# Kernel optimization log

Hardware: AMD Instinct MI355X
Metric: run time of the kernel (lower is better)

Reference implementation:

```python
import jax, jax.numpy as jnp
import numpy as np

C = 256
DQK = C // 8


def setup_inputs() -> dict:
    key = jax.random.key(0)
    ks = jax.random.split(key, 7)
    B, H, W = 8, 64, 64
    x = jax.random.normal(ks[0], (B, H, W, C), dtype=jnp.float32)
    # 1x1 conv weights (equivalent to per-pixel dense): [Cin, Cout] + bias
    sq = 1.0 / np.sqrt(C)
    Wq = jax.random.normal(ks[1], (C, DQK), dtype=jnp.float32) * sq
    bq = jnp.zeros((DQK,), dtype=jnp.float32)
    Wk = jax.random.normal(ks[2], (C, DQK), dtype=jnp.float32) * sq
    bk = jnp.zeros((DQK,), dtype=jnp.float32)
    Wv = jax.random.normal(ks[3], (C, C), dtype=jnp.float32) * sq
    bv = jnp.zeros((C,), dtype=jnp.float32)
    gamma = jnp.float32(0.5)  # nonzero so attention path affects output/grads
    return {"x": x, "Wq": Wq, "bq": bq, "Wk": Wk, "bk": bk,
            "Wv": Wv, "bv": bv, "gamma": gamma}


def reference(x, Wq, bq, Wk, bk, Wv, bv, gamma):
    B, H, W, c = x.shape
    n = H * W
    xf = x.reshape(B, n, c)                      # [B, hw, C]
    q = xf @ Wq + bq                              # [B, hw, C//8]
    k = xf @ Wk + bk                              # [B, hw, C//8]
    v = xf @ Wv + bv                              # [B, hw, C]
    scores = jnp.einsum('bnd,bmd->bnm', q, k)     # [B, hw, hw], no scaling (faithful)
    attn = jax.nn.softmax(scores, axis=-1)
    out = jnp.einsum('bnm,bmc->bnc', attn, v)     # [B, hw, C]
    out = out.reshape(B, H, W, c)
    return gamma * out + x
```

## Files before the change

### kernel.cpp

```cpp
#include <hip/hip_runtime.h>
#include <hip/hip_bf16.h>
#include <math.h>

#define B_ 8
#define N_ 4096
#define C_ 256
#define DQK_ 32

typedef float f32x4  __attribute__((ext_vector_type(4)));
typedef float f32x16 __attribute__((ext_vector_type(16)));
typedef short bf16x8 __attribute__((ext_vector_type(8)));
typedef short bf16x4 __attribute__((ext_vector_type(4)));

__device__ __forceinline__ short f2bf(float f){
  union { float f; unsigned u; } v; v.f = f;
  unsigned r = v.u + 0x7fffu + ((v.u >> 16) & 1u);
  return (short)(r >> 16);
}

__global__ void cast_wt_kernel(const float* __restrict__ Wq, const float* __restrict__ Wk,
                               const float* __restrict__ Wv, short* __restrict__ WT){
  int n = blockIdx.x;
  int k = threadIdx.x;
  float val;
  if (n < 32)       val = Wq[k*32 + n];
  else if (n < 64)  val = Wk[k*32 + (n-32)];
  else              val = Wv[k*256 + (n-64)];
  WT[n*256 + k] = f2bf(val);
}

__global__ __launch_bounds__(256) void proj_kernel(
    const float* __restrict__ x, const short* __restrict__ WT,
    const float* __restrict__ bq, const float* __restrict__ bk, const float* __restrict__ bv,
    short* __restrict__ qws, short* __restrict__ kws, short* __restrict__ vSw){
  __shared__ __align__(16) short sX[64*264];
  __shared__ __align__(16) short sT[64*72];
  int tid = threadIdx.x;
  int lane = tid & 63, wave = tid >> 6;
  int lane15 = lane & 15, quad = lane >> 4;
  int mbase = blockIdx.x * 64;
  int b = mbase >> 12, kvb = mbase & (N_-1);

  const float* xr = x + (size_t)mbase * C_;
  for (int i = 0; i < 8; i++){
    int s = tid + i*256;
    int row = s >> 5, cg = (s & 31) << 3;
    const f32x4* src = (const f32x4*)(xr + row*C_ + cg);
    f32x4 a = src[0], c = src[1];
    bf16x8 p;
    p[0]=f2bf(a[0]); p[1]=f2bf(a[1]); p[2]=f2bf(a[2]); p[3]=f2bf(a[3]);
    p[4]=f2bf(c[0]); p[5]=f2bf(c[1]); p[6]=f2bf(c[2]); p[7]=f2bf(c[3]);
    *(bf16x8*)(sX + row*264 + cg) = p;
  }
  __syncthreads();

  f32x4 acc[5][4];
  for (int i=0;i<5;i++) for (int mt=0;mt<4;mt++) acc[i][mt] = (f32x4)(0.f);

  for (int kc = 0; kc < 8; kc++){
    bf16x8 afr[4];
    #pragma unroll
    for (int mt=0;mt<4;mt++)
      afr[mt] = *(const bf16x8*)(sX + (mt*16+lane15)*264 + kc*32 + quad*8);
    bf16x8 bfr[5];
    #pragma unroll
    for (int i=0;i<5;i++){
      int t = i*4 + wave;
      bfr[i] = *(const bf16x8*)(WT + (size_t)(t*16+lane15)*256 + kc*32 + quad*8);
    }
    #pragma unroll
    for (int i=0;i<5;i++)
      #pragma unroll
      for (int mt=0;mt<4;mt++)
        acc[i][mt] = __builtin_amdgcn_mfma_f32_16x16x32_bf16(afr[mt], bfr[i], acc[i][mt], 0,0,0);
  }

  #pragma unroll
  for (int i=0;i<5;i++){
    int t = i*4 + wave;
    int n0 = t*16 + lane15;
    float bias = (n0 < 32) ? bq[n0] : (n0 < 64 ? bk[n0-32] : bv[n0-64]);
    if (n0 < 64){
      #pragma unroll
      for (int mt=0;mt<4;mt++)
        #pragma unroll
        for (int r=0;r<4;r++)
          sT[(mt*16 + quad*4 + r)*72 + n0] = f2bf(acc[i][mt][r] + bias);
    } else {
      int ch = n0 - 64, cht = ch >> 5, c5 = ch & 31;
      int lanep = c5 | ((quad & 1) << 5);
      int jo = (quad >> 1) * 4;
      #pragma unroll
      for (int mt=0;mt<4;mt++){
        bf16x4 pk;
        pk[0]=f2bf(acc[i][mt][0]+bias); pk[1]=f2bf(acc[i][mt][1]+bias);
        pk[2]=f2bf(acc[i][mt][2]+bias); pk[3]=f2bf(acc[i][mt][3]+bias);
        size_t off = (size_t)b*1048576 + (size_t)(kvb>>6)*16384
                   + (size_t)(mt*8 + cht)*512 + (size_t)lanep*8 + jo;
        *(bf16x4*)(vSw + off) = pk;
      }
    }
  }
  __syncthreads();

  {
    int qt = tid >> 7, p = (tid >> 6) & 1, ln = tid & 63;
    int row = qt*32 + (ln & 31);
    int dcol = p*16 + (ln >> 5)*8;
    bf16x8 vq = *(const bf16x8*)(sT + row*72 + dcol);
    bf16x8 vk = *(const bf16x8*)(sT + row*72 + 32 + dcol);
    size_t qoff = ((((size_t)b*128 + ((kvb>>5) + qt))*2 + p)*64 + ln)*8;
    *(bf16x8*)(qws + qoff) = vq;
    size_t koff = ((size_t)b*64 + (kvb>>6))*2048 + (size_t)((qt*2 + p)*64 + ln)*8;
    *(bf16x8*)(kws + koff) = vk;
  }
}

__global__ __launch_bounds__(512, 2) void flash_kernel(
    const float* __restrict__ x, const short* __restrict__ qws, const short* __restrict__ kws,
    const short* __restrict__ vSw, const float* __restrict__ gptr, float* __restrict__ out){
  __shared__ __align__(16) char smem[98304];
  short* sV0 = (short*)smem;
  short* sV1 = (short*)(smem + 32768);
  int tid = threadIdx.x;
  int lane = tid & 63, wave = tid >> 6;
  int l31 = lane & 31, h = lane >> 5;
  int qt = wave >> 1, kh = wave & 1;
  int b = blockIdx.x & 7;
  int q0 = (blockIdx.x >> 3) << 7;

  const short* qb = qws + (size_t)b*131072;
  const short* kb = kws + (size_t)b*131072;
  const short* vb = vSw + (size_t)b*1048576;

  int qtg = (q0 >> 5) + qt;
  bf16x8 qf0 = *(const bf16x8*)(qb + (size_t)((qtg*2+0)*64 + lane)*8);
  bf16x8 qf1 = *(const bf16x8*)(qb + (size_t)((qtg*2+1)*64 + lane)*8);

  const short* kf0p = kb + (size_t)((2*kh+0)*64 + lane)*8;
  const short* kf1p = kb + (size_t)((2*kh+1)*64 + lane)*8;
  bf16x8 kfc0 = *(const bf16x8*)(kf0p);
  bf16x8 kfc1 = *(const bf16x8*)(kf1p);
  bf16x8 kfn0 = kfc0, kfn1 = kfc1;

  #pragma unroll
  for (int r=0;r<4;r++)
    __builtin_amdgcn_global_load_lds(
      (const __attribute__((address_space(1))) void*)(vb + (size_t)(r*512+tid)*8),
      (__attribute__((address_space(3))) void*)(sV0 + (size_t)(r*512+tid)*8), 16, 0, 0);
  __syncthreads();

  f32x16 acc[8], accl;
  #pragma unroll
  for (int t=0;t<8;t++) acc[t] = (f32x16)(0.f);
  accl = (f32x16)(0.f);
  bf16x8 ones;
  #pragma unroll
  for (int j=0;j<8;j++) ones[j] = (short)0x3F80;

  for (int it=0; it<64; it++){
    short* sVc = (it & 1) ? sV1 : sV0;
    short* sVn = (it & 1) ? sV0 : sV1;
    if (it < 63){
      const short* vsrc = vb + (size_t)(it+1)*16384;
      #pragma unroll
      for (int r=0;r<4;r++)
        __builtin_amdgcn_global_load_lds(
          (const __attribute__((address_space(1))) void*)(vsrc + (size_t)(r*512+tid)*8),
          (__attribute__((address_space(3))) void*)(sVn + (size_t)(r*512+tid)*8), 16, 0, 0);
      kfn0 = *(const bf16x8*)(kf0p + (size_t)(it+1)*2048);
      kfn1 = *(const bf16x8*)(kf1p + (size_t)(it+1)*2048);
    }

    f32x16 s = __builtin_amdgcn_mfma_f32_32x32x16_bf16(kfc0, qf0, (f32x16)(0.f), 0,0,0);
    s        = __builtin_amdgcn_mfma_f32_32x32x16_bf16(kfc1, qf1, s, 0,0,0);

    bf16x8 pf[2];
    #pragma unroll
    for (int g=0; g<2; g++){
      union { bf16x8 v; unsigned u[4]; } P;
      #pragma unroll
      for (int j=0;j<4;j++){
        float2 e;
        e.x = __expf(s[g*8 + 2*j]);
        e.y = __expf(s[g*8 + 2*j + 1]);
        __hip_bfloat162 t2 = __float22bfloat162_rn(e);
        __builtin_memcpy(&P.u[j], &t2, 4);
      }
      pf[g] = P.v;
    }

    #pragma unroll
    for (int g=0; g<2; g++){
      const short* base = sVc + (2*kh + g)*4096;
      #pragma unroll
      for (int cht=0; cht<8; cht++){
        bf16x8 vf = *(const bf16x8*)(base + (cht*64 + lane)*8);
        acc[cht] = __builtin_amdgcn_mfma_f32_32x32x16_bf16(pf[g], vf, acc[cht], 0,0,0);
      }
      accl = __builtin_amdgcn_mfma_f32_32x32x16_bf16(pf[g], ones, accl, 0,0,0);
    }
    kfc0 = kfn0; kfc1 = kfn1;
    __syncthreads();
  }

  float* R1 = (float*)smem;
  float* RL = (float*)(smem + 65536);
  int pw = wave ^ 1;
  if (kh == 0){
    #pragma unroll
    for (int i=0;i<16;i++){ R1[wave*2048 + i*64 + lane] = acc[4][i];
                            R1[wave*2048 + 1024 + i*64 + lane] = acc[5][i]; }
  } else {
    #pragma unroll
    for (int i=0;i<16;i++){ R1[wave*2048 + i*64 + lane] = acc[0][i];
                            R1[wave*2048 + 1024 + i*64 + lane] = acc[1][i]; }
  }
  #pragma unroll
  for (int i=0;i<16;i++) RL[wave*1024 + i*64 + lane] = accl[i];
  __syncthreads();
  if (kh == 0){
    #pragma unroll
    for (int i=0;i<16;i++){ acc[0][i] += R1[pw*2048 + i*64 + lane];
                            acc[1][i] += R1[pw*2048 + 1024 + i*64 + lane]; }
  } else {
    #pragma unroll
    for (int i=0;i<16;i++){ acc[4][i] += R1[pw*2048 + i*64 + lane];
                            acc[5][i] += R1[pw*2048 + 1024 + i*64 + lane]; }
  }
  #pragma unroll
  for (int i=0;i<16;i++) accl[i] += RL[pw*1024 + i*64 + lane];
  __syncthreads();
  if (kh == 0){
    #pragma unroll
    for (int i=0;i<16;i++){ R1[wave*2048 + i*64 + lane] = acc[6][i];
                            R1[wave*2048 + 1024 + i*64 + lane] = acc[7][i]; }
  } else {
    #pragma unroll
    for (int i=0;i<16;i++){ R1[wave*2048 + i*64 + lane] = acc[2][i];
                            R1[wave*2048 + 1024 + i*64 + lane] = acc[3][i]; }
  }
  __syncthreads();
  if (kh == 0){
    #pragma unroll
    for (int i=0;i<16;i++){ acc[2][i] += R1[pw*2048 + i*64 + lane];
                            acc[3][i] += R1[pw*2048 + 1024 + i*64 + lane]; }
  } else {
    #pragma unroll
    for (int i=0;i<16;i++){ acc[6][i] += R1[pw*2048 + i*64 + lane];
                            acc[7][i] += R1[pw*2048 + 1024 + i*64 + lane]; }
  }

  float g = *gptr;
  const float* xb = x + ((size_t)b*N_ + q0 + qt*32)*C_;
  float*       ob = out + ((size_t)b*N_ + q0 + qt*32)*C_;
  if (kh == 0){
    #pragma unroll
    for (int i=0;i<16;i++){
      int q = (i&3) + 8*(i>>2) + 4*h;
      float rv = 1.f / accl[i];
      #pragma unroll
      for (int ct=0; ct<4; ct++){
        int ch = ct*32 + l31;
        ob[(size_t)q*C_ + ch] = g*(acc[ct][i]*rv) + xb[(size_t)q*C_ + ch];
      }
    }
  } else {
    #pragma unroll
    for (int i=0;i<16;i++){
      int q = (i&3) + 8*(i>>2) + 4*h;
      float rv = 1.f / accl[i];
      #pragma unroll
      for (int ct=0; ct<4; ct++){
        int ch = (4+ct)*32 + l31;
        ob[(size_t)q*C_ + ch] = g*(acc[4+ct][i]*rv) + xb[(size_t)q*C_ + ch];
      }
    }
  }
}

extern "C" void kernel_launch(void* const* d_in, const int* in_sizes, int n_in,
                              void* d_out, int out_size, void* d_ws, size_t ws_size,
                              hipStream_t stream){
  const float* x  = (const float*)d_in[0];
  const float* Wq = (const float*)d_in[1];
  const float* bq = (const float*)d_in[2];
  const float* Wk = (const float*)d_in[3];
  const float* bk = (const float*)d_in[4];
  const float* Wv = (const float*)d_in[5];
  const float* bv = (const float*)d_in[6];
  const float* gm = (const float*)d_in[7];
  float* out = (float*)d_out;
  char* ws = (char*)d_ws;
  short* WT  = (short*)ws;
  short* qws = (short*)(ws + 163840);
  short* kws = (short*)(ws + 163840 + 2097152);
  short* vSw = (short*)(ws + 163840 + 2*2097152);

  cast_wt_kernel<<<dim3(320), dim3(256), 0, stream>>>(Wq, Wk, Wv, WT);
  proj_kernel<<<dim3(512), dim3(256), 0, stream>>>(x, WT, bq, bk, bv, qws, kws, vSw);
  flash_kernel<<<dim3(256), dim3(512), 0, stream>>>(x, qws, kws, vSw, gm, out);
}
```

Measured before the change: 188.6 us.

## Software-pipeline QK scores one step ahead and compute row sums on VALU

Unrolls the KV loop by two with explicit ping-pong buffers so the next tile's QK^T MFMAs are issued alongside the current tile's exp and PV MFMAs. It also drops the extra MFMA against a ones vector, accumulating softmax row sums in scalar registers and reducing them through a small shared table. Shared memory shrinks to about 65 KB, which may help occupancy. The cost is more live registers and more complex control flow. The row-sum mapping relies on the MFMA output lane layout, where each lane's s values belong to a single query column.

```diff
diff --git a/kernel.cpp b/kernel.cpp
--- a/kernel.cpp
+++ b/kernel.cpp
@@ -119,7 +119,7 @@
 __global__ __launch_bounds__(512, 2) void flash_kernel(
     const float* __restrict__ x, const short* __restrict__ qws, const short* __restrict__ kws,
     const short* __restrict__ vSw, const float* __restrict__ gptr, float* __restrict__ out){
-  __shared__ __align__(16) char smem[98304];
+  __shared__ __align__(16) char smem[66560];
   short* sV0 = (short*)smem;
   short* sV1 = (short*)(smem + 32768);
   int tid = threadIdx.x;
@@ -139,74 +139,103 @@
 
   const short* kf0p = kb + (size_t)((2*kh+0)*64 + lane)*8;
   const short* kf1p = kb + (size_t)((2*kh+1)*64 + lane)*8;
-  bf16x8 kfc0 = *(const bf16x8*)(kf0p);
-  bf16x8 kfc1 = *(const bf16x8*)(kf1p);
-  bf16x8 kfn0 = kfc0, kfn1 = kfc1;
-
-  #pragma unroll
-  for (int r=0;r<4;r++)
-    __builtin_amdgcn_global_load_lds(
-      (const __attribute__((address_space(1))) void*)(vb + (size_t)(r*512+tid)*8),
-      (__attribute__((address_space(3))) void*)(sV0 + (size_t)(r*512+tid)*8), 16, 0, 0);
-  __syncthreads();
-
-  f32x16 acc[8], accl;
+  bf16x8 kA0 = *(const bf16x8*)(kf0p);
+  bf16x8 kA1 = *(const bf16x8*)(kf1p);
+  bf16x8 kB0 = *(const bf16x8*)(kf0p + 2048);
+  bf16x8 kB1 = *(const bf16x8*)(kf1p + 2048);
+
+#define VPREF(CHUNK, DST) do { \
+    const short* vsrc_ = vb + (size_t)(CHUNK)*16384; \
+    _Pragma("unroll") \
+    for (int r_=0;r_<4;r_++) \
+      __builtin_amdgcn_global_load_lds( \
+        (const __attribute__((address_space(1))) void*)(vsrc_ + (size_t)(r_*512+tid)*8), \
+        (__attribute__((address_space(3))) void*)((DST) + (size_t)(r_*512+tid)*8), 16, 0, 0); \
+  } while(0)
+
+#define QKS(K0, K1) ({ \
+    f32x16 t_ = __builtin_amdgcn_mfma_f32_32x32x16_bf16((K0), qf0, (f32x16)(0.f), 0,0,0); \
+    __builtin_amdgcn_mfma_f32_32x32x16_bf16((K1), qf1, t_, 0,0,0); })
+
+#define EXPPACK(S, PF) do { \
+    float ls_ = 0.f; \
+    _Pragma("unroll") \
+    for (int g_=0; g_<2; g_++){ \
+      union { bf16x8 v; unsigned u[4]; } P_; \
+      _Pragma("unroll") \
+      for (int j_=0;j_<4;j_++){ \
+        float2 e_; \
+        e_.x = __expf((S)[g_*8 + 2*j_]); \
+        e_.y = __expf((S)[g_*8 + 2*j_ + 1]); \
+        ls_ += e_.x + e_.y; \
+        __hip_bfloat162 t2_ = __float22bfloat162_rn(e_); \
+        __builtin_memcpy(&P_.u[j_], &t2_, 4); \
+      } \
+      (PF)[g_] = P_.v; \
+    } \
+    rsum += ls_; \
+  } while(0)
+
+#define PV_STEP(SVC, PF) do { \
+    _Pragma("unroll") \
+    for (int g_=0; g_<2; g_++){ \
+      const short* base_ = (SVC) + (2*kh + g_)*4096; \
+      _Pragma("unroll") \
+      for (int cht_=0; cht_<8; cht_++){ \
+        bf16x8 vf_ = *(const bf16x8*)(base_ + (cht_*64 + lane)*8); \
+        acc[cht_] = __builtin_amdgcn_mfma_f32_32x32x16_bf16((PF)[g_], vf_, acc[cht_], 0,0,0); \
+      } \
+    } \
+  } while(0)
+
+  VPREF(0, sV0);
+  __syncthreads();
+
+  f32x16 acc[8];
   #pragma unroll
   for (int t=0;t<8;t++) acc[t] = (f32x16)(0.f);
-  accl = (f32x16)(0.f);
-  bf16x8 ones;
-  #pragma unroll
-  for (int j=0;j<8;j++) ones[j] = (short)0x3F80;
-
-  for (int it=0; it<64; it++){
-    short* sVc = (it & 1) ? sV1 : sV0;
-    short* sVn = (it & 1) ? sV0 : sV1;
-    if (it < 63){
-      const short* vsrc = vb + (size_t)(it+1)*16384;
-      #pragma unroll
-      for (int r=0;r<4;r++)
-        __builtin_amdgcn_global_load_lds(
-          (const __attribute__((address_space(1))) void*)(vsrc + (size_t)(r*512+tid)*8),
-          (__attribute__((address_space(3))) void*)(sVn + (size_t)(r*512+tid)*8), 16, 0, 0);
-      kfn0 = *(const bf16x8*)(kf0p + (size_t)(it+1)*2048);
-      kfn1 = *(const bf16x8*)(kf1p + (size_t)(it+1)*2048);
-    }
-
-    f32x16 s = __builtin_amdgcn_mfma_f32_32x32x16_bf16(kfc0, qf0, (f32x16)(0.f), 0,0,0);
-    s        = __builtin_amdgcn_mfma_f32_32x32x16_bf16(kfc1, qf1, s, 0,0,0);
-
-    bf16x8 pf[2];
-    #pragma unroll
-    for (int g=0; g<2; g++){
-      union { bf16x8 v; unsigned u[4]; } P;
-      #pragma unroll
-      for (int j=0;j<4;j++){
-        float2 e;
-        e.x = __expf(s[g*8 + 2*j]);
-        e.y = __expf(s[g*8 + 2*j + 1]);
-        __hip_bfloat162 t2 = __float22bfloat162_rn(e);
-        __builtin_memcpy(&P.u[j], &t2, 4);
-      }
-      pf[g] = P.v;
-    }
-
-    #pragma unroll
-    for (int g=0; g<2; g++){
-      const short* base = sVc + (2*kh + g)*4096;
-      #pragma unroll
-      for (int cht=0; cht<8; cht++){
-        bf16x8 vf = *(const bf16x8*)(base + (cht*64 + lane)*8);
-        acc[cht] = __builtin_amdgcn_mfma_f32_32x32x16_bf16(pf[g], vf, acc[cht], 0,0,0);
-      }
-      accl = __builtin_amdgcn_mfma_f32_32x32x16_bf16(pf[g], ones, accl, 0,0,0);
-    }
-    kfc0 = kfn0; kfc1 = kfn1;
-    __syncthreads();
+  float rsum = 0.f;
+
+  f32x16 s0 = QKS(kA0, kA1);
+  f32x16 s1 = (f32x16)(0.f);
+  kA0 = *(const bf16x8*)(kf0p + 2*2048);
+  kA1 = *(const bf16x8*)(kf1p + 2*2048);
+
+  for (int it2 = 0; it2 < 32; it2++){
+    {
+      VPREF(2*it2+1, sV1);
+      bf16x8 pf[2];
+      EXPPACK(s0, pf);
+      s1 = QKS(kB0, kB1);
+      if (it2 < 31){
+        kB0 = *(const bf16x8*)(kf0p + (size_t)(2*it2+3)*2048);
+        kB1 = *(const bf16x8*)(kf1p + (size_t)(2*it2+3)*2048);
+      }
+      PV_STEP(sV0, pf);
+      __syncthreads();
+    }
+    {
+      if (it2 < 31) VPREF(2*it2+2, sV0);
+      bf16x8 pf[2];
+      EXPPACK(s1, pf);
+      if (it2 < 31){
+        s0 = QKS(kA0, kA1);
+        if (it2 < 30){
+          kA0 = *(const bf16x8*)(kf0p + (size_t)(2*it2+4)*2048);
+          kA1 = *(const bf16x8*)(kf1p + (size_t)(2*it2+4)*2048);
+        }
+      }
+      PV_STEP(sV1, pf);
+      __syncthreads();
+    }
   }
 
   float* R1 = (float*)smem;
-  float* RL = (float*)(smem + 65536);
+  float* TAB = (float*)(smem + 65536);
   int pw = wave ^ 1;
+  rsum += __shfl_xor(rsum, 32);
+  if (lane < 32) TAB[wave*32 + lane] = rsum;
+
   if (kh == 0){
     #pragma unroll
     for (int i=0;i<16;i++){ R1[wave*2048 + i*64 + lane] = acc[4][i];
@@ -216,8 +245,6 @@
     for (int i=0;i<16;i++){ R1[wave*2048 + i*64 + lane] = acc[0][i];
                             R1[wave*2048 + 1024 + i*64 + lane] = acc[1][i]; }
   }
-  #pragma unroll
-  for (int i=0;i<16;i++) RL[wave*1024 + i*64 + lane] = accl[i];
   __syncthreads();
   if (kh == 0){
     #pragma unroll
@@ -228,8 +255,6 @@
     for (int i=0;i<16;i++){ acc[4][i] += R1[pw*2048 + i*64 + lane];
                             acc[5][i] += R1[pw*2048 + 1024 + i*64 + lane]; }
   }
-  #pragma unroll
-  for (int i=0;i<16;i++) accl[i] += RL[pw*1024 + i*64 + lane];
   __syncthreads();
   if (kh == 0){
     #pragma unroll
@@ -258,7 +283,7 @@
     #pragma unroll
     for (int i=0;i<16;i++){
       int q = (i&3) + 8*(i>>2) + 4*h;
-      float rv = 1.f / accl[i];
+      float rv = 1.f / (TAB[(qt*2+0)*32 + q] + TAB[(qt*2+1)*32 + q]);
       #pragma unroll
       for (int ct=0; ct<4; ct++){
         int ch = ct*32 + l31;
@@ -269,7 +294,7 @@
     #pragma unroll
     for (int i=0;i<16;i++){
       int q = (i&3) + 8*(i>>2) + 4*h;
-      float rv = 1.f / accl[i];
+      float rv = 1.f / (TAB[(qt*2+0)*32 + q] + TAB[(qt*2+1)*32 + q]);
       #pragma unroll
       for (int ct=0; ct<4; ct++){
         int ch = (4+ct)*32 + l31;
@@ -277,6 +302,10 @@
       }
     }
   }
+#undef VPREF
+#undef QKS
+#undef EXPPACK
+#undef PV_STEP
 }
 
 extern "C" void kernel_launch(void* const* d_in, const int* in_sizes, int n_in,
```

Measured after the change: 191.6 us. No clear change (+1.6%).

## Deepen V prefetch to four LDS buffers and compute row sums in VALU

Applied to the files above, without the earlier changes.

Changes the V staging from a double buffer to a four-slot LDS ring with a two-iteration prefetch distance. Each iteration now waits with a manual vmcnt and one raw s_barrier instead of a full __syncthreads. The softmax denominator is no longer an extra MFMA against a ones vector; it is accumulated as a scalar sum of the exponentials, reduced across lanes and waves in LDS, which removes two MFMAs per iteration. The LDS footprint grows to 128KB per block, which may cut occupancy below the two blocks per CU that launch_bounds asks for. The hand-tuned vmcnt counts could also be fragile.

```diff
diff --git a/kernel.cpp b/kernel.cpp
--- a/kernel.cpp
+++ b/kernel.cpp
@@ -119,9 +119,7 @@
 __global__ __launch_bounds__(512, 2) void flash_kernel(
     const float* __restrict__ x, const short* __restrict__ qws, const short* __restrict__ kws,
     const short* __restrict__ vSw, const float* __restrict__ gptr, float* __restrict__ out){
-  __shared__ __align__(16) char smem[98304];
-  short* sV0 = (short*)smem;
-  short* sV1 = (short*)(smem + 32768);
+  __shared__ __align__(16) char smem[131072];
   int tid = threadIdx.x;
   int lane = tid & 63, wave = tid >> 6;
   int l31 = lane & 31, h = lane >> 5;
@@ -139,42 +137,41 @@
 
   const short* kf0p = kb + (size_t)((2*kh+0)*64 + lane)*8;
   const short* kf1p = kb + (size_t)((2*kh+1)*64 + lane)*8;
+
+#define VPREF(CHUNK, DST) do { \
+    const short* vsrc_ = vb + (size_t)(CHUNK)*16384; \
+    _Pragma("unroll") \
+    for (int r_=0;r_<4;r_++) \
+      __builtin_amdgcn_global_load_lds( \
+        (const __attribute__((address_space(1))) void*)(vsrc_ + (size_t)(r_*512+tid)*8), \
+        (__attribute__((address_space(3))) void*)((DST) + (size_t)(r_*512+tid)*8), 16, 0, 0); \
+  } while(0)
+
+  VPREF(0, (short*)smem);
+  VPREF(1, (short*)(smem + 32768));
+  __builtin_amdgcn_sched_barrier(0);
   bf16x8 kfc0 = *(const bf16x8*)(kf0p);
   bf16x8 kfc1 = *(const bf16x8*)(kf1p);
-  bf16x8 kfn0 = kfc0, kfn1 = kfc1;
-
-  #pragma unroll
-  for (int r=0;r<4;r++)
-    __builtin_amdgcn_global_load_lds(
-      (const __attribute__((address_space(1))) void*)(vb + (size_t)(r*512+tid)*8),
-      (__attribute__((address_space(3))) void*)(sV0 + (size_t)(r*512+tid)*8), 16, 0, 0);
-  __syncthreads();
-
-  f32x16 acc[8], accl;
+  __builtin_amdgcn_sched_barrier(0);
+  bf16x8 kfn0, kfn1;
+
+  f32x16 acc[8];
   #pragma unroll
   for (int t=0;t<8;t++) acc[t] = (f32x16)(0.f);
-  accl = (f32x16)(0.f);
-  bf16x8 ones;
-  #pragma unroll
-  for (int j=0;j<8;j++) ones[j] = (short)0x3F80;
+  float rsO = 0.f;
 
   for (int it=0; it<64; it++){
-    short* sVc = (it & 1) ? sV1 : sV0;
-    short* sVn = (it & 1) ? sV0 : sV1;
-    if (it < 63){
-      const short* vsrc = vb + (size_t)(it+1)*16384;
-      #pragma unroll
-      for (int r=0;r<4;r++)
-        __builtin_amdgcn_global_load_lds(
-          (const __attribute__((address_space(1))) void*)(vsrc + (size_t)(r*512+tid)*8),
-          (__attribute__((address_space(3))) void*)(sVn + (size_t)(r*512+tid)*8), 16, 0, 0);
-      kfn0 = *(const bf16x8*)(kf0p + (size_t)(it+1)*2048);
-      kfn1 = *(const bf16x8*)(kf1p + (size_t)(it+1)*2048);
-    }
+    int nk = (it+1 < 64) ? (it+1) : 63;
+    int ns = (it+2 < 64) ? (it+2) : 63;
+
+    kfn0 = *(const bf16x8*)(kf0p + (size_t)nk*2048);
+    kfn1 = *(const bf16x8*)(kf1p + (size_t)nk*2048);
+    __builtin_amdgcn_sched_barrier(0);
+    VPREF(ns, (short*)(smem + ((size_t)((it+2)&3))*32768));
+    __builtin_amdgcn_sched_barrier(0);
 
     f32x16 s = __builtin_amdgcn_mfma_f32_32x32x16_bf16(kfc0, qf0, (f32x16)(0.f), 0,0,0);
     s        = __builtin_amdgcn_mfma_f32_32x32x16_bf16(kfc1, qf1, s, 0,0,0);
-
     bf16x8 pf[2];
     #pragma unroll
     for (int g=0; g<2; g++){
@@ -184,29 +181,44 @@
         float2 e;
         e.x = __expf(s[g*8 + 2*j]);
         e.y = __expf(s[g*8 + 2*j + 1]);
+        rsO += e.x + e.y;
         __hip_bfloat162 t2 = __float22bfloat162_rn(e);
         __builtin_memcpy(&P.u[j], &t2, 4);
       }
       pf[g] = P.v;
     }
 
-    #pragma unroll
-    for (int g=0; g<2; g++){
-      const short* base = sVc + (2*kh + g)*4096;
-      #pragma unroll
-      for (int cht=0; cht<8; cht++){
-        bf16x8 vf = *(const bf16x8*)(base + (cht*64 + lane)*8);
-        acc[cht] = __builtin_amdgcn_mfma_f32_32x32x16_bf16(pf[g], vf, acc[cht], 0,0,0);
-      }
-      accl = __builtin_amdgcn_mfma_f32_32x32x16_bf16(pf[g], ones, accl, 0,0,0);
+    asm volatile("s_waitcnt vmcnt(4)" ::: "memory");
+    __builtin_amdgcn_sched_barrier(0);
+    __builtin_amdgcn_s_barrier();
+    __builtin_amdgcn_sched_barrier(0);
+
+    {
+      const short* sVc = (const short*)(smem + ((size_t)(it&3))*32768);
+      #pragma unroll
+      for (int g=0; g<2; g++){
+        const short* base = sVc + (2*kh + g)*4096;
+        #pragma unroll
+        for (int cht=0; cht<8; cht++){
+          bf16x8 vf = *(const bf16x8*)(base + (cht*64 + lane)*8);
+          acc[cht] = __builtin_amdgcn_mfma_f32_32x32x16_bf16(pf[g], vf, acc[cht], 0,0,0);
+        }
+      }
     }
     kfc0 = kfn0; kfc1 = kfn1;
-    __syncthreads();
-  }
-
+  }
+
+  asm volatile("s_waitcnt vmcnt(0)" ::: "memory");
+  __builtin_amdgcn_sched_barrier(0);
+  __builtin_amdgcn_s_barrier();
+  __builtin_amdgcn_sched_barrier(0);
+
+  rsO += __shfl_xor(rsO, 32);
   float* R1 = (float*)smem;
-  float* RL = (float*)(smem + 65536);
+  float* RS = (float*)(smem + 65536);
   int pw = wave ^ 1;
+  if (lane < 32) RS[wave*32 + l31] = rsO;
+
   if (kh == 0){
     #pragma unroll
     for (int i=0;i<16;i++){ R1[wave*2048 + i*64 + lane] = acc[4][i];
@@ -216,8 +228,6 @@
     for (int i=0;i<16;i++){ R1[wave*2048 + i*64 + lane] = acc[0][i];
                             R1[wave*2048 + 1024 + i*64 + lane] = acc[1][i]; }
   }
-  #pragma unroll
-  for (int i=0;i<16;i++) RL[wave*1024 + i*64 + lane] = accl[i];
   __syncthreads();
   if (kh == 0){
     #pragma unroll
@@ -228,8 +238,6 @@
     for (int i=0;i<16;i++){ acc[4][i] += R1[pw*2048 + i*64 + lane];
                             acc[5][i] += R1[pw*2048 + 1024 + i*64 + lane]; }
   }
-  #pragma unroll
-  for (int i=0;i<16;i++) accl[i] += RL[pw*1024 + i*64 + lane];
   __syncthreads();
   if (kh == 0){
     #pragma unroll
@@ -258,7 +266,7 @@
     #pragma unroll
     for (int i=0;i<16;i++){
       int q = (i&3) + 8*(i>>2) + 4*h;
-      float rv = 1.f / accl[i];
+      float rv = 1.f / (RS[(qt*2+0)*32 + q] + RS[(qt*2+1)*32 + q]);
       #pragma unroll
       for (int ct=0; ct<4; ct++){
         int ch = ct*32 + l31;
@@ -269,7 +277,7 @@
     #pragma unroll
     for (int i=0;i<16;i++){
       int q = (i&3) + 8*(i>>2) + 4*h;
-      float rv = 1.f / accl[i];
+      float rv = 1.f / (RS[(qt*2+0)*32 + q] + RS[(qt*2+1)*32 + q]);
       #pragma unroll
       for (int ct=0; ct<4; ct++){
         int ch = (4+ct)*32 + l31;
@@ -277,6 +285,7 @@
       }
     }
   }
+#undef VPREF
 }
 
 extern "C" void kernel_launch(void* const* d_in, const int* in_sizes, int n_in,
```

Result: slower. 194.4 us (+3.1%).
